# Performance work log

Measured on AMD Instinct MI355X. Metric: run time of the kernel, lower is better.

Reference implementation:

```python
import jax, jax.numpy as jnp
import numpy as np

B, D, H = 512, 256, 512

def setup_inputs() -> dict:
    key = jax.random.key(0)
    ks = jax.random.split(key, 7)
    s = lambda fan_in: 1.0 / np.sqrt(fan_in)
    return {
        "h": jax.random.normal(ks[0], (B, D), jnp.float32),
        "W1": jax.random.normal(ks[1], (2 * D, H), jnp.float32) * s(2 * D),
        "b1": jax.random.normal(ks[2], (H,), jnp.float32) * s(2 * D),
        "W2": jax.random.normal(ks[3], (H, H), jnp.float32) * s(H),
        "b2": jax.random.normal(ks[4], (H,), jnp.float32) * s(H),
        "W3": jax.random.normal(ks[5], (H, 1), jnp.float32) * s(H),
        "b3": jax.random.normal(ks[6], (1,), jnp.float32) * s(H),
    }

def reference(h, W1, b1, W2, b2, W3, b3):
    n = h.shape[0]
    # Split W1 into halves acting on hi and hj; equivalent to cat([hi,hj]) @ W1
    yi = h @ W1[:D]            # [B, H]
    yj = h @ W1[D:]            # [B, H]
    x = jnp.tanh(yi[:, None, :] + yj[None, :, :] + b1)   # [B, B, H]
    x = jnp.tanh(x @ W2 + b2)                             # [B, B, H]
    logits = (x @ W3 + b3)[..., 0]                        # [B, B]
    eye = jnp.eye(n, dtype=logits.dtype)
    return logits * (1.0 - eye) + (-20.0) * eye
```

## Files before the change

### kernel.cpp

```cpp
#include <hip/hip_runtime.h>
#include <cstdint>


#define NB 512
#define ND 256
#define NH 512
#define C2 2.885390081777927f

typedef int i32x4 __attribute__((ext_vector_type(4)));
typedef int i32x16 __attribute__((ext_vector_type(16)));
typedef unsigned int u32;
typedef unsigned char u8;

__device__ __forceinline__ float exp2_fast(float x) {
#if __has_builtin(__builtin_amdgcn_exp2f)
  return __builtin_amdgcn_exp2f(x);
#else
  return exp2f(x);
#endif
}
__device__ __forceinline__ float rcp_fast(float x) {
#if __has_builtin(__builtin_amdgcn_rcpf)
  return __builtin_amdgcn_rcpf(x);
#else
  return 1.0f / x;
#endif
}
__device__ __forceinline__ u32 perm_b32(u32 hi, u32 lo, u32 sel) {
#if __has_builtin(__builtin_amdgcn_perm)
  return __builtin_amdgcn_perm(hi, lo, sel);
#else
  u32 r = 0;
  for (int b = 0; b < 4; ++b) {
    const u32 c = (sel >> (8 * b)) & 255;
    const u32 byte = (c < 4) ? (lo >> (8 * c)) & 255 : (c < 8) ? (hi >> (8 * (c - 4))) & 255 : 0;
    r |= byte << (8 * b);
  }
  return r;
#endif
}
__device__ __forceinline__ u32 tanh_q127_magic(float u) {
  const float r = rcp_fast(exp2_fast(u) + 1.0f);
  return __builtin_bit_cast(u32, fmaf(-254.0f, r, 12583039.0f));
}

__global__ __launch_bounds__(256) void prep_all(const float* __restrict__ h,
                                                const float* __restrict__ W1,
                                                const float* __restrict__ b1,
                                                const float* __restrict__ W2,
                                                float* __restrict__ Ai,
                                                float* __restrict__ Aj,
                                                u8* __restrict__ W2q) {
  const int t = threadIdx.x;
  const int bx = blockIdx.x;
  if (bx < 256) {
    __shared__ float hsh[4][ND];
    const int i0 = (bx >> 1) * 4;
    const int n = (bx & 1) * 256 + t;
#pragma unroll
    for (int ii = 0; ii < 4; ++ii) hsh[ii][t] = h[(i0 + ii) * ND + t];
    __syncthreads();
    float ai[4] = {0.0f, 0.0f, 0.0f, 0.0f};
    float aj[4] = {0.0f, 0.0f, 0.0f, 0.0f};
#pragma unroll 4
    for (int d = 0; d < ND; ++d) {
      const float wa = W1[d * NH + n];
      const float wb = W1[(d + ND) * NH + n];
#pragma unroll
      for (int ii = 0; ii < 4; ++ii) {
        const float hd = hsh[ii][d];
        ai[ii] = fmaf(hd, wa, ai[ii]);
        aj[ii] = fmaf(hd, wb, aj[ii]);
      }
    }
    const float b1n = b1[n];
#pragma unroll
    for (int ii = 0; ii < 4; ++ii) {
      Ai[(i0 + ii) * NH + n] = ai[ii] * C2;
      Aj[(i0 + ii) * NH + n] = (aj[ii] + b1n) * C2;
    }
  } else {
    const int g = (bx - 256) * 256 + t;
    const int lane = g & 63;
    const int nt = (g >> 6) & 15;
    const int ks = g >> 10;
    const int n = nt * 32 + (lane & 31);
    const int kb = ks * 32 + ((lane >> 5) << 4);
    u32 w[4];
#pragma unroll
    for (int q = 0; q < 4; ++q) {
      u32 acc = 0;
#pragma unroll
      for (int j = 0; j < 4; ++j) {
        const float wv = fminf(fmaxf(W2[(kb + q * 4 + j) * NH + n], -0.25f), 0.25f);
        const int qi = (int)rintf(wv * 508.0f);
        acc |= ((u32)(qi & 255)) << (8 * j);
      }
      w[q] = acc;
    }
    ((uint4*)W2q)[g] = make_uint4(w[0], w[1], w[2], w[3]);
  }
}

__global__ __launch_bounds__(1024, 8) void pair_main(const float* __restrict__ Ai,
                                                     const float* __restrict__ Aj,
                                                     const u8* __restrict__ W2q,
                                                     const float* __restrict__ b2,
                                                     const float* __restrict__ W3,
                                                     const float* __restrict__ b3,
                                                     float* __restrict__ out) {
  __shared__ __align__(16) u8 xs[64 * 512];
  __shared__ float red[16][32];

  const int t = threadIdx.x;
  const int w = t >> 6;
  const int lane = t & 63;
  const int lhi = lane >> 5;
  const int llo = lane & 31;
  const int wn = w & 7;
  const int mh = w >> 3;
  const int bx = blockIdx.x;
  const int i = bx >> 3;
  const int j0 = (bx & 7) * 64;

  i32x16 acc[2];
#pragma unroll
  for (int nt = 0; nt < 2; ++nt)
#pragma unroll
    for (int q = 0; q < 16; ++q) acc[nt][q] = 0;

  {
    const int row = t & 63;
    const int s0 = t >> 6;
    const float* ajr = Aj + (size_t)(j0 + row) * NH;
    const float* air = Ai + (size_t)i * NH;
#pragma unroll
    for (int uu = 0; uu < 2; ++uu) {
      const int s = s0 + uu * 16;
      const int k0 = s * 16;
      u32 wds[4];
#pragma unroll
      for (int q = 0; q < 4; ++q) {
        const float4 fa = *(const float4*)(ajr + k0 + q * 4);
        const float4 ga = *(const float4*)(air + k0 + q * 4);
        const u32 m0 = tanh_q127_magic(fa.x + ga.x);
        const u32 m1 = tanh_q127_magic(fa.y + ga.y);
        const u32 m2 = tanh_q127_magic(fa.z + ga.z);
        const u32 m3 = tanh_q127_magic(fa.w + ga.w);
        const u32 p01 = perm_b32(m1, m0, 0x0C0C0400u);
        const u32 p23 = perm_b32(m3, m2, 0x0C0C0400u);
        wds[q] = perm_b32(p23, p01, 0x05040100u);
      }
      ((uint4*)xs)[s * 64 + row] = make_uint4(wds[0], wds[1], wds[2], wds[3]);
    }
  }
  __syncthreads();

  const i32x4* xsv = (const i32x4*)xs;
  const int abase = lhi * 64 + mh * 32 + llo;
  const uint4* w2v = (const uint4*)W2q + wn * 128 + lane;

  i32x4 aP0 = xsv[abase];
  i32x4 aP1 = xsv[128 + abase];
  uint4 bP00 = w2v[0], bP01 = w2v[64];
  uint4 bP10 = w2v[1024], bP11 = w2v[1024 + 64];

#pragma unroll
  for (int kk = 0; kk < 8; ++kk) {
    const int ks0 = 2 * kk;
    {
      const i32x4 a = aP0;
      const i32x4 c0 = __builtin_bit_cast(i32x4, bP00);
      const i32x4 c1 = __builtin_bit_cast(i32x4, bP01);
      if (kk < 7) {
        aP0 = xsv[(ks0 + 2) * 128 + abase];
        const uint4* wp = w2v + (ks0 + 2) * 1024;
        bP00 = wp[0];
        bP01 = wp[64];
      }
      acc[0] = __builtin_amdgcn_mfma_i32_32x32x32_i8(a, c0, acc[0], 0, 0, 0);
      acc[1] = __builtin_amdgcn_mfma_i32_32x32x32_i8(a, c1, acc[1], 0, 0, 0);
    }
    {
      const i32x4 a = aP1;
      const i32x4 c0 = __builtin_bit_cast(i32x4, bP10);
      const i32x4 c1 = __builtin_bit_cast(i32x4, bP11);
      if (kk < 7) {
        aP1 = xsv[(ks0 + 3) * 128 + abase];
        const uint4* wp = w2v + (ks0 + 3) * 1024;
        bP10 = wp[0];
        bP11 = wp[64];
      }
      acc[0] = __builtin_amdgcn_mfma_i32_32x32x32_i8(a, c0, acc[0], 0, 0, 0);
      acc[1] = __builtin_amdgcn_mfma_i32_32x32x32_i8(a, c1, acc[1], 0, 0, 0);
    }
  }

  const float SCALE = (0.25f / (127.0f * 127.0f)) * C2;
  float b2c[2], w3v[2];
#pragma unroll
  for (int ntl = 0; ntl < 2; ++ntl) {
    const int n = wn * 64 + ntl * 32 + llo;
    b2c[ntl] = b2[n] * C2;
    w3v[ntl] = W3[n];
  }
  float w3s = w3v[0] + w3v[1];
#pragma unroll
  for (int off = 1; off < 32; off <<= 1) w3s += __shfl_xor(w3s, off, 64);

#pragma unroll
  for (int reg = 0; reg < 16; ++reg) {
    float sr = 0.0f;
#pragma unroll
    for (int ntl = 0; ntl < 2; ++ntl) {
      const float y = fmaf((float)acc[ntl][reg], SCALE, b2c[ntl]);
      const float r = rcp_fast(exp2_fast(y) + 1.0f);
      sr = fmaf(w3v[ntl], r, sr);
    }
#pragma unroll
    for (int off = 1; off < 32; off <<= 1) sr += __shfl_xor(sr, off, 64);
    const int row = (reg & 3) + 8 * (reg >> 2) + 4 * lhi;
    if (llo == reg) red[w][row] = fmaf(-2.0f, sr, w3s);
  }
  __syncthreads();
  if (t < 64) {
    const int mh2 = t >> 5;
    const int rl = t & 31;
    float v = b3[0];
#pragma unroll
    for (int ww = 0; ww < 8; ++ww) v += red[mh2 * 8 + ww][rl];
    const int j = j0 + t;
    out[i * NB + j] = (j == i) ? -20.0f : v;
  }
}

extern "C" void kernel_launch(void* const* d_in, const int* in_sizes, int n_in,
                              void* d_out, int out_size, void* d_ws, size_t ws_size,
                              hipStream_t stream) {
  const float* h = (const float*)d_in[0];
  const float* W1 = (const float*)d_in[1];
  const float* b1 = (const float*)d_in[2];
  const float* W2 = (const float*)d_in[3];
  const float* b2 = (const float*)d_in[4];
  const float* W3 = (const float*)d_in[5];
  const float* b3 = (const float*)d_in[6];
  float* out = (float*)d_out;

  float* Ai = (float*)d_ws;
  float* Aj = Ai + NB * NH;
  u8* W2q = (u8*)(Aj + NB * NH);

  prep_all<<<320, 256, 0, stream>>>(h, W1, b1, W2, Ai, Aj, W2q);
  pair_main<<<4096, 1024, 0, stream>>>(Ai, Aj, W2q, b2, W3, b3, out);
}
```

Baseline: 248.2 us.

## Make pair kernel persistent with register-resident W2 and double-buffered LDS tiles

Each block now handles 32 rows of i against a 32-wide j tile, looping over i. The quantized W2 fragments are loaded once into registers and reused across all iterations, and the Aj slice is also held in registers. The next row's tanh-quantized activations are packed into a second LDS buffer while the current MFMA and epilogue run, and the output reduction is deferred one iteration. This removes the per-block W2 reloads and launch overhead of 4096 blocks, at the cost of only 256 blocks, heavy register use (128 VGPRs just for W2) and fewer waves to hide latency.

```diff
diff --git a/kernel.cpp b/kernel.cpp
--- a/kernel.cpp
+++ b/kernel.cpp
@@ -42,6 +42,21 @@
 __device__ __forceinline__ u32 tanh_q127_magic(float u) {
   const float r = rcp_fast(exp2_fast(u) + 1.0f);
   return __builtin_bit_cast(u32, fmaf(-254.0f, r, 12583039.0f));
+}
+
+__device__ __forceinline__ uint4 pack16(const float4* fa, const float4* ga) {
+  u32 wds[4];
+#pragma unroll
+  for (int q = 0; q < 4; ++q) {
+    const u32 m0 = tanh_q127_magic(fa[q].x + ga[q].x);
+    const u32 m1 = tanh_q127_magic(fa[q].y + ga[q].y);
+    const u32 m2 = tanh_q127_magic(fa[q].z + ga[q].z);
+    const u32 m3 = tanh_q127_magic(fa[q].w + ga[q].w);
+    const u32 p01 = perm_b32(m1, m0, 0x0C0C0400u);
+    const u32 p23 = perm_b32(m3, m2, 0x0C0C0400u);
+    wds[q] = perm_b32(p23, p01, 0x05040100u);
+  }
+  return make_uint4(wds[0], wds[1], wds[2], wds[3]);
 }
 
 __global__ __launch_bounds__(256) void prep_all(const float* __restrict__ h,
@@ -102,97 +117,34 @@
   }
 }
 
-__global__ __launch_bounds__(1024, 8) void pair_main(const float* __restrict__ Ai,
-                                                     const float* __restrict__ Aj,
-                                                     const u8* __restrict__ W2q,
-                                                     const float* __restrict__ b2,
-                                                     const float* __restrict__ W3,
-                                                     const float* __restrict__ b3,
-                                                     float* __restrict__ out) {
-  __shared__ __align__(16) u8 xs[64 * 512];
-  __shared__ float red[16][32];
+__global__ __launch_bounds__(512, 2) void pair_main(const float* __restrict__ Ai,
+                                                    const float* __restrict__ Aj,
+                                                    const u8* __restrict__ W2q,
+                                                    const float* __restrict__ b2,
+                                                    const float* __restrict__ W3,
+                                                    const float* __restrict__ b3,
+                                                    float* __restrict__ out) {
+  __shared__ __align__(16) u8 xs[2][32 * 512];
+  __shared__ float red[2][8][32];
 
   const int t = threadIdx.x;
   const int w = t >> 6;
   const int lane = t & 63;
   const int lhi = lane >> 5;
   const int llo = lane & 31;
-  const int wn = w & 7;
-  const int mh = w >> 3;
   const int bx = blockIdx.x;
-  const int i = bx >> 3;
-  const int j0 = (bx & 7) * 64;
-
-  i32x16 acc[2];
-#pragma unroll
-  for (int nt = 0; nt < 2; ++nt)
-#pragma unroll
-    for (int q = 0; q < 16; ++q) acc[nt][q] = 0;
-
+  const int jt = bx & 15;
+  const int ich = bx >> 4;
+  const int j0 = jt * 32;
+  const int i0 = ich * 32;
+
+  i32x4 Bf[16][2];
   {
-    const int row = t & 63;
-    const int s0 = t >> 6;
-    const float* ajr = Aj + (size_t)(j0 + row) * NH;
-    const float* air = Ai + (size_t)i * NH;
-#pragma unroll
-    for (int uu = 0; uu < 2; ++uu) {
-      const int s = s0 + uu * 16;
-      const int k0 = s * 16;
-      u32 wds[4];
-#pragma unroll
-      for (int q = 0; q < 4; ++q) {
-        const float4 fa = *(const float4*)(ajr + k0 + q * 4);
-        const float4 ga = *(const float4*)(air + k0 + q * 4);
-        const u32 m0 = tanh_q127_magic(fa.x + ga.x);
-        const u32 m1 = tanh_q127_magic(fa.y + ga.y);
-        const u32 m2 = tanh_q127_magic(fa.z + ga.z);
-        const u32 m3 = tanh_q127_magic(fa.w + ga.w);
-        const u32 p01 = perm_b32(m1, m0, 0x0C0C0400u);
-        const u32 p23 = perm_b32(m3, m2, 0x0C0C0400u);
-        wds[q] = perm_b32(p23, p01, 0x05040100u);
-      }
-      ((uint4*)xs)[s * 64 + row] = make_uint4(wds[0], wds[1], wds[2], wds[3]);
-    }
-  }
-  __syncthreads();
-
-  const i32x4* xsv = (const i32x4*)xs;
-  const int abase = lhi * 64 + mh * 32 + llo;
-  const uint4* w2v = (const uint4*)W2q + wn * 128 + lane;
-
-  i32x4 aP0 = xsv[abase];
-  i32x4 aP1 = xsv[128 + abase];
-  uint4 bP00 = w2v[0], bP01 = w2v[64];
-  uint4 bP10 = w2v[1024], bP11 = w2v[1024 + 64];
-
-#pragma unroll
-  for (int kk = 0; kk < 8; ++kk) {
-    const int ks0 = 2 * kk;
-    {
-      const i32x4 a = aP0;
-      const i32x4 c0 = __builtin_bit_cast(i32x4, bP00);
-      const i32x4 c1 = __builtin_bit_cast(i32x4, bP01);
-      if (kk < 7) {
-        aP0 = xsv[(ks0 + 2) * 128 + abase];
-        const uint4* wp = w2v + (ks0 + 2) * 1024;
-        bP00 = wp[0];
-        bP01 = wp[64];
-      }
-      acc[0] = __builtin_amdgcn_mfma_i32_32x32x32_i8(a, c0, acc[0], 0, 0, 0);
-      acc[1] = __builtin_amdgcn_mfma_i32_32x32x32_i8(a, c1, acc[1], 0, 0, 0);
-    }
-    {
-      const i32x4 a = aP1;
-      const i32x4 c0 = __builtin_bit_cast(i32x4, bP10);
-      const i32x4 c1 = __builtin_bit_cast(i32x4, bP11);
-      if (kk < 7) {
-        aP1 = xsv[(ks0 + 3) * 128 + abase];
-        const uint4* wp = w2v + (ks0 + 3) * 1024;
-        bP10 = wp[0];
-        bP11 = wp[64];
-      }
-      acc[0] = __builtin_amdgcn_mfma_i32_32x32x32_i8(a, c0, acc[0], 0, 0, 0);
-      acc[1] = __builtin_amdgcn_mfma_i32_32x32x32_i8(a, c1, acc[1], 0, 0, 0);
+    const uint4* w2v = (const uint4*)W2q + w * 128 + lane;
+#pragma unroll
+    for (int ks = 0; ks < 16; ++ks) {
+      Bf[ks][0] = __builtin_bit_cast(i32x4, w2v[ks * 1024]);
+      Bf[ks][1] = __builtin_bit_cast(i32x4, w2v[ks * 1024 + 64]);
     }
   }
 
@@ -200,37 +152,112 @@
   float b2c[2], w3v[2];
 #pragma unroll
   for (int ntl = 0; ntl < 2; ++ntl) {
-    const int n = wn * 64 + ntl * 32 + llo;
+    const int n = w * 64 + ntl * 32 + llo;
     b2c[ntl] = b2[n] * C2;
     w3v[ntl] = W3[n];
   }
   float w3s = w3v[0] + w3v[1];
 #pragma unroll
   for (int off = 1; off < 32; off <<= 1) w3s += __shfl_xor(w3s, off, 64);
-
-#pragma unroll
-  for (int reg = 0; reg < 16; ++reg) {
-    float sr = 0.0f;
-#pragma unroll
-    for (int ntl = 0; ntl < 2; ++ntl) {
-      const float y = fmaf((float)acc[ntl][reg], SCALE, b2c[ntl]);
-      const float r = rcp_fast(exp2_fast(y) + 1.0f);
-      sr = fmaf(w3v[ntl], r, sr);
-    }
-#pragma unroll
-    for (int off = 1; off < 32; off <<= 1) sr += __shfl_xor(sr, off, 64);
-    const int row = (reg & 3) + 8 * (reg >> 2) + 4 * lhi;
-    if (llo == reg) red[w][row] = fmaf(-2.0f, sr, w3s);
+  const float b3v = b3[0];
+
+  const int srow = t & 31;
+  const int ss0 = t >> 5;
+  const int k0 = ss0 * 16;
+
+  float4 fj[8];
+  {
+    const float* ajr = Aj + (size_t)(j0 + srow) * NH;
+#pragma unroll
+    for (int q = 0; q < 4; ++q) {
+      fj[q] = *(const float4*)(ajr + k0 + q * 4);
+      fj[q + 4] = *(const float4*)(ajr + k0 + 256 + q * 4);
+    }
+  }
+
+  {
+    const float* air = Ai + (size_t)i0 * NH;
+    float4 gi[8];
+#pragma unroll
+    for (int q = 0; q < 4; ++q) {
+      gi[q] = *(const float4*)(air + k0 + q * 4);
+      gi[q + 4] = *(const float4*)(air + k0 + 256 + q * 4);
+    }
+    ((uint4*)xs[0])[ss0 * 32 + srow] = pack16(fj, gi);
+    ((uint4*)xs[0])[(ss0 + 16) * 32 + srow] = pack16(fj + 4, gi + 4);
   }
   __syncthreads();
-  if (t < 64) {
-    const int mh2 = t >> 5;
-    const int rl = t & 31;
-    float v = b3[0];
-#pragma unroll
-    for (int ww = 0; ww < 8; ++ww) v += red[mh2 * 8 + ww][rl];
+
+  const int abase = lhi * 32 + llo;
+
+  for (int il = 0; il < 32; ++il) {
+    const int buf = il & 1;
+    const int i = i0 + il;
+
+    float4 gi[8];
+    if (il < 31) {
+      const float* air = Ai + (size_t)(i + 1) * NH;
+#pragma unroll
+      for (int q = 0; q < 4; ++q) {
+        gi[q] = *(const float4*)(air + k0 + q * 4);
+        gi[q + 4] = *(const float4*)(air + k0 + 256 + q * 4);
+      }
+    }
+
+    i32x16 acc[2];
+#pragma unroll
+    for (int ntl = 0; ntl < 2; ++ntl)
+#pragma unroll
+      for (int q = 0; q < 16; ++q) acc[ntl][q] = 0;
+    {
+      const i32x4* xv = (const i32x4*)(xs[buf]);
+#pragma unroll
+      for (int ks = 0; ks < 16; ++ks) {
+        const i32x4 a = xv[ks * 64 + abase];
+        acc[0] = __builtin_amdgcn_mfma_i32_32x32x32_i8(a, Bf[ks][0], acc[0], 0, 0, 0);
+        acc[1] = __builtin_amdgcn_mfma_i32_32x32x32_i8(a, Bf[ks][1], acc[1], 0, 0, 0);
+      }
+    }
+
+    if (il < 31) {
+      ((uint4*)xs[buf ^ 1])[ss0 * 32 + srow] = pack16(fj, gi);
+      ((uint4*)xs[buf ^ 1])[(ss0 + 16) * 32 + srow] = pack16(fj + 4, gi + 4);
+    }
+
+#pragma unroll
+    for (int reg = 0; reg < 16; ++reg) {
+      float sr = 0.0f;
+#pragma unroll
+      for (int ntl = 0; ntl < 2; ++ntl) {
+        const float y = fmaf((float)acc[ntl][reg], SCALE, b2c[ntl]);
+        const float r = rcp_fast(exp2_fast(y) + 1.0f);
+        sr = fmaf(w3v[ntl], r, sr);
+      }
+#pragma unroll
+      for (int off = 1; off < 32; off <<= 1) sr += __shfl_xor(sr, off, 64);
+      const int row = (reg & 3) + 8 * (reg >> 2) + 4 * lhi;
+      if (llo == reg) red[buf][w][row] = fmaf(-2.0f, sr, w3s);
+    }
+
+    if (il > 0 && t < 32) {
+      float v = b3v;
+#pragma unroll
+      for (int ww = 0; ww < 8; ++ww) v += red[buf ^ 1][ww][t];
+      const int ip = i - 1;
+      const int j = j0 + t;
+      out[ip * NB + j] = (j == ip) ? -20.0f : v;
+    }
+
+    __syncthreads();
+  }
+
+  if (t < 32) {
+    float v = b3v;
+#pragma unroll
+    for (int ww = 0; ww < 8; ++ww) v += red[1][ww][t];
+    const int ip = i0 + 31;
     const int j = j0 + t;
-    out[i * NB + j] = (j == i) ? -20.0f : v;
+    out[ip * NB + j] = (j == ip) ? -20.0f : v;
   }
 }
 
@@ -251,5 +278,5 @@
   u8* W2q = (u8*)(Aj + NB * NH);
 
   prep_all<<<320, 256, 0, stream>>>(h, W1, b1, W2, Ai, Aj, W2q);
-  pair_main<<<4096, 1024, 0, stream>>>(Ai, Aj, W2q, b2, W3, b3, out);
-}
+  pair_main<<<256, 512, 0, stream>>>(Ai, Aj, W2q, b2, W3, b3, out);
+}
```

Result: slower. 267.6 us (+7.8%).

## Halve pair tile to 32 rows, batch transcendentals, restructure epilogue reduction

Applied to the files above, without the earlier changes.

The pair kernel now uses 512-thread blocks covering 32 j-rows (8192 blocks) instead of 1024-thread blocks covering 64 rows. The tanh-to-int8 staging and the layer-2 tanh are batched so all exp2 and rcp calls are issued together. The cross-lane reduction becomes a short shuffle plus a shared-memory transpose and a 16-lane reduce. Smaller blocks are meant to improve scheduling and cut the long 32-step shuffle chain. The cost is W2q fragments being loaded twice as often per output row and higher register pressure from the batched arrays.

```diff
diff --git a/kernel.cpp b/kernel.cpp
--- a/kernel.cpp
+++ b/kernel.cpp
@@ -38,10 +38,6 @@
   }
   return r;
 #endif
-}
-__device__ __forceinline__ u32 tanh_q127_magic(float u) {
-  const float r = rcp_fast(exp2_fast(u) + 1.0f);
-  return __builtin_bit_cast(u32, fmaf(-254.0f, r, 12583039.0f));
 }
 
 __global__ __launch_bounds__(256) void prep_all(const float* __restrict__ h,
@@ -102,26 +98,76 @@
   }
 }
 
-__global__ __launch_bounds__(1024, 8) void pair_main(const float* __restrict__ Ai,
-                                                     const float* __restrict__ Aj,
-                                                     const u8* __restrict__ W2q,
-                                                     const float* __restrict__ b2,
-                                                     const float* __restrict__ W3,
-                                                     const float* __restrict__ b3,
-                                                     float* __restrict__ out) {
-  __shared__ __align__(16) u8 xs[64 * 512];
-  __shared__ float red[16][32];
+__global__ __launch_bounds__(512, 4) void pair_main(const float* __restrict__ Ai,
+                                                    const float* __restrict__ Aj,
+                                                    const u8* __restrict__ W2q,
+                                                    const float* __restrict__ b2,
+                                                    const float* __restrict__ W3,
+                                                    const float* __restrict__ b3,
+                                                    float* __restrict__ out) {
+  __shared__ __align__(16) u8 xs[32 * 512];
+  __shared__ float red2[32][64];
+  __shared__ float wsum[8];
 
   const int t = threadIdx.x;
   const int w = t >> 6;
   const int lane = t & 63;
   const int lhi = lane >> 5;
   const int llo = lane & 31;
-  const int wn = w & 7;
-  const int mh = w >> 3;
   const int bx = blockIdx.x;
-  const int i = bx >> 3;
-  const int j0 = (bx & 7) * 64;
+  const int i = bx >> 4;
+  const int j0 = (bx & 15) * 32;
+
+  const float SCALE = (0.25f / (127.0f * 127.0f)) * C2;
+  float b2c[2], w3v[2];
+#pragma unroll
+  for (int ntl = 0; ntl < 2; ++ntl) {
+    const int n = w * 64 + ntl * 32 + llo;
+    b2c[ntl] = b2[n] * C2;
+    w3v[ntl] = W3[n];
+  }
+  {
+    float w3s = w3v[0] + w3v[1];
+#pragma unroll
+    for (int off = 1; off < 32; off <<= 1) w3s += __shfl_xor(w3s, off, 64);
+    if (lane == 0) wsum[w] = w3s;
+  }
+
+  {
+    const int srow = t & 31;
+    const int ss0 = t >> 5;
+    const int k0 = ss0 * 16;
+    const float* ajr = Aj + (size_t)(j0 + srow) * NH;
+    const float* air = Ai + (size_t)i * NH;
+    float s[32];
+#pragma unroll
+    for (int g = 0; g < 8; ++g) {
+      const int ko = k0 + (g & 3) * 4 + (g >> 2) * 256;
+      const float4 fa = *(const float4*)(ajr + ko);
+      const float4 ga = *(const float4*)(air + ko);
+      s[g * 4 + 0] = fa.x + ga.x;
+      s[g * 4 + 1] = fa.y + ga.y;
+      s[g * 4 + 2] = fa.z + ga.z;
+      s[g * 4 + 3] = fa.w + ga.w;
+    }
+#pragma unroll
+    for (int q = 0; q < 32; ++q) s[q] = exp2_fast(s[q]);
+#pragma unroll
+    for (int q = 0; q < 32; ++q) s[q] = rcp_fast(s[q] + 1.0f);
+    u32 m[32];
+#pragma unroll
+    for (int q = 0; q < 32; ++q) m[q] = __builtin_bit_cast(u32, fmaf(-254.0f, s[q], 12583039.0f));
+    u32 wd[8];
+#pragma unroll
+    for (int g = 0; g < 8; ++g) {
+      const u32 p01 = perm_b32(m[g * 4 + 1], m[g * 4 + 0], 0x0C0C0400u);
+      const u32 p23 = perm_b32(m[g * 4 + 3], m[g * 4 + 2], 0x0C0C0400u);
+      wd[g] = perm_b32(p23, p01, 0x05040100u);
+    }
+    ((uint4*)xs)[ss0 * 32 + srow] = make_uint4(wd[0], wd[1], wd[2], wd[3]);
+    ((uint4*)xs)[(ss0 + 16) * 32 + srow] = make_uint4(wd[4], wd[5], wd[6], wd[7]);
+  }
+  __syncthreads();
 
   i32x16 acc[2];
 #pragma unroll
@@ -129,39 +175,12 @@
 #pragma unroll
     for (int q = 0; q < 16; ++q) acc[nt][q] = 0;
 
-  {
-    const int row = t & 63;
-    const int s0 = t >> 6;
-    const float* ajr = Aj + (size_t)(j0 + row) * NH;
-    const float* air = Ai + (size_t)i * NH;
-#pragma unroll
-    for (int uu = 0; uu < 2; ++uu) {
-      const int s = s0 + uu * 16;
-      const int k0 = s * 16;
-      u32 wds[4];
-#pragma unroll
-      for (int q = 0; q < 4; ++q) {
-        const float4 fa = *(const float4*)(ajr + k0 + q * 4);
-        const float4 ga = *(const float4*)(air + k0 + q * 4);
-        const u32 m0 = tanh_q127_magic(fa.x + ga.x);
-        const u32 m1 = tanh_q127_magic(fa.y + ga.y);
-        const u32 m2 = tanh_q127_magic(fa.z + ga.z);
-        const u32 m3 = tanh_q127_magic(fa.w + ga.w);
-        const u32 p01 = perm_b32(m1, m0, 0x0C0C0400u);
-        const u32 p23 = perm_b32(m3, m2, 0x0C0C0400u);
-        wds[q] = perm_b32(p23, p01, 0x05040100u);
-      }
-      ((uint4*)xs)[s * 64 + row] = make_uint4(wds[0], wds[1], wds[2], wds[3]);
-    }
-  }
-  __syncthreads();
-
   const i32x4* xsv = (const i32x4*)xs;
-  const int abase = lhi * 64 + mh * 32 + llo;
-  const uint4* w2v = (const uint4*)W2q + wn * 128 + lane;
+  const int abase = lhi * 32 + llo;
+  const uint4* w2v = (const uint4*)W2q + w * 128 + lane;
 
   i32x4 aP0 = xsv[abase];
-  i32x4 aP1 = xsv[128 + abase];
+  i32x4 aP1 = xsv[64 + abase];
   uint4 bP00 = w2v[0], bP01 = w2v[64];
   uint4 bP10 = w2v[1024], bP11 = w2v[1024 + 64];
 
@@ -173,7 +192,7 @@
       const i32x4 c0 = __builtin_bit_cast(i32x4, bP00);
       const i32x4 c1 = __builtin_bit_cast(i32x4, bP01);
       if (kk < 7) {
-        aP0 = xsv[(ks0 + 2) * 128 + abase];
+        aP0 = xsv[(ks0 + 2) * 64 + abase];
         const uint4* wp = w2v + (ks0 + 2) * 1024;
         bP00 = wp[0];
         bP01 = wp[64];
@@ -186,7 +205,7 @@
       const i32x4 c0 = __builtin_bit_cast(i32x4, bP10);
       const i32x4 c1 = __builtin_bit_cast(i32x4, bP11);
       if (kk < 7) {
-        aP1 = xsv[(ks0 + 3) * 128 + abase];
+        aP1 = xsv[(ks0 + 3) * 64 + abase];
         const uint4* wp = w2v + (ks0 + 3) * 1024;
         bP10 = wp[0];
         bP11 = wp[64];
@@ -196,41 +215,42 @@
     }
   }
 
-  const float SCALE = (0.25f / (127.0f * 127.0f)) * C2;
-  float b2c[2], w3v[2];
-#pragma unroll
-  for (int ntl = 0; ntl < 2; ++ntl) {
-    const int n = wn * 64 + ntl * 32 + llo;
-    b2c[ntl] = b2[n] * C2;
-    w3v[ntl] = W3[n];
-  }
-  float w3s = w3v[0] + w3v[1];
-#pragma unroll
-  for (int off = 1; off < 32; off <<= 1) w3s += __shfl_xor(w3s, off, 64);
-
+  float ev[32];
 #pragma unroll
   for (int reg = 0; reg < 16; ++reg) {
-    float sr = 0.0f;
-#pragma unroll
-    for (int ntl = 0; ntl < 2; ++ntl) {
-      const float y = fmaf((float)acc[ntl][reg], SCALE, b2c[ntl]);
-      const float r = rcp_fast(exp2_fast(y) + 1.0f);
-      sr = fmaf(w3v[ntl], r, sr);
-    }
-#pragma unroll
-    for (int off = 1; off < 32; off <<= 1) sr += __shfl_xor(sr, off, 64);
+    ev[reg] = fmaf((float)acc[0][reg], SCALE, b2c[0]);
+    ev[16 + reg] = fmaf((float)acc[1][reg], SCALE, b2c[1]);
+  }
+#pragma unroll
+  for (int q = 0; q < 32; ++q) ev[q] = exp2_fast(ev[q]);
+#pragma unroll
+  for (int q = 0; q < 32; ++q) ev[q] = rcp_fast(ev[q] + 1.0f);
+
+#pragma unroll
+  for (int reg = 0; reg < 16; ++reg) {
+    float sr = fmaf(w3v[0], ev[reg], w3v[1] * ev[16 + reg]);
+    sr += __shfl_xor(sr, 1, 64);
+    sr += __shfl_xor(sr, 2, 64);
     const int row = (reg & 3) + 8 * (reg >> 2) + 4 * lhi;
-    if (llo == reg) red[w][row] = fmaf(-2.0f, sr, w3s);
+    if ((llo & 3) == 0) red2[row][w * 8 + (llo >> 2)] = sr;
   }
   __syncthreads();
-  if (t < 64) {
-    const int mh2 = t >> 5;
-    const int rl = t & 31;
-    float v = b3[0];
-#pragma unroll
-    for (int ww = 0; ww < 8; ++ww) v += red[mh2 * 8 + ww][rl];
-    const int j = j0 + t;
-    out[i * NB + j] = (j == i) ? -20.0f : v;
+
+  {
+    const float w3tot = b3[0] + ((wsum[0] + wsum[1]) + (wsum[2] + wsum[3])) +
+                        ((wsum[4] + wsum[5]) + (wsum[6] + wsum[7]));
+    const int row = t >> 4;
+    const int sub = t & 15;
+    const float4 v = *(const float4*)&red2[row][sub * 4];
+    float s2 = (v.x + v.y) + (v.z + v.w);
+    s2 += __shfl_xor(s2, 1, 16);
+    s2 += __shfl_xor(s2, 2, 16);
+    s2 += __shfl_xor(s2, 4, 16);
+    s2 += __shfl_xor(s2, 8, 16);
+    if (sub == 0) {
+      const int j = j0 + row;
+      out[i * NB + j] = (j == i) ? -20.0f : fmaf(-2.0f, s2, w3tot);
+    }
   }
 }
 
@@ -251,5 +271,5 @@
   u8* W2q = (u8*)(Aj + NB * NH);
 
   prep_all<<<320, 256, 0, stream>>>(h, W1, b1, W2, Ai, Aj, W2q);
-  pair_main<<<4096, 1024, 0, stream>>>(Ai, Aj, W2q, b2, W3, b3, out);
-}
+  pair_main<<<8192, 512, 0, stream>>>(Ai, Aj, W2q, b2, W3, b3, out);
+}
```

After: 246.0 us. Within noise of the previous version (-0.9%).
